# Performance work log

Hardware: AMD Instinct MI355X
Metric: run time of the kernel (lower is better)

Reference implementation:

```python
import jax, jax.numpy as jnp
import numpy as np

E = 1024   # embed_dim
H = 16     # num_heads
DH = E // H
FF = 4096  # intermediate_size
EPS = 1e-5


def layernorm(x, g, b):
    mu = jnp.mean(x, axis=-1, keepdims=True)
    var = jnp.var(x, axis=-1, keepdims=True)
    return (x - mu) * jax.lax.rsqrt(var + EPS) * g + b


def setup_inputs() -> dict:
    key = jax.random.key(0)
    ks = jax.random.split(key, 16)
    s = 0.02
    return {
        "x": jax.random.normal(ks[0], (2, 2048, E), dtype=jnp.float32),
        "ln1_g": jnp.ones((E,), jnp.float32),
        "ln1_b": jnp.zeros((E,), jnp.float32),
        "ln2_g": jnp.ones((E,), jnp.float32),
        "ln2_b": jnp.zeros((E,), jnp.float32),
        # per-head Q/K/V projections stacked: [H, E, DH]
        "wq": jax.random.normal(ks[1], (H, E, DH), jnp.float32) * s,
        "bq": jnp.zeros((H, DH), jnp.float32),
        "wk": jax.random.normal(ks[2], (H, E, DH), jnp.float32) * s,
        "bk": jnp.zeros((H, DH), jnp.float32),
        "wv": jax.random.normal(ks[3], (H, E, DH), jnp.float32) * s,
        "bv": jnp.zeros((H, DH), jnp.float32),
        "wo": jax.random.normal(ks[4], (E, E), jnp.float32) * s,
        "bo": jnp.zeros((E,), jnp.float32),
        "w1": jax.random.normal(ks[5], (E, FF), jnp.float32) * s,
        "b1": jnp.zeros((FF,), jnp.float32),
        "w2": jax.random.normal(ks[6], (FF, E), jnp.float32) * s,
        "b2": jnp.zeros((E,), jnp.float32),
    }


def reference(x, ln1_g, ln1_b, ln2_g, ln2_b, wq, bq, wk, bk, wv, bv,
              wo, bo, w1, b1, w2, b2):
    # --- multi-head attention (pre-LN) ---
    h = layernorm(x, ln1_g, ln1_b)                       # [B,S,E]
    q = jnp.einsum('bse,hed->bhsd', h, wq) + bq[:, None, :]
    k = jnp.einsum('bse,hed->bhsd', h, wk) + bk[:, None, :]
    v = jnp.einsum('bse,hed->bhsd', h, wv) + bv[:, None, :]
    scores = jnp.einsum('bhsd,bhtd->bhst', q, k) / jnp.sqrt(
        jnp.asarray(DH, x.dtype))                        # [B,H,S,S]
    w = jax.nn.softmax(scores, axis=-1)
    attn = jnp.einsum('bhst,bhtd->bhsd', w, v)           # [B,H,S,DH]
    B, _, S, _ = attn.shape
    concat = attn.transpose(0, 2, 1, 3).reshape(B, S, E)  # head concat order
    x = x + concat @ wo + bo
    # --- feed-forward (pre-LN), exact GELU, dropout_p=0 ---
    h2 = layernorm(x, ln2_g, ln2_b)
    ff = jax.nn.gelu(h2 @ w1 + b1, approximate=False) @ w2 + b2
    return x + ff
```

## Files before the change

### kernel.cpp

```cpp
#include <hip/hip_runtime.h>
#include <hip/hip_bf16.h>
#include <math.h>

typedef __attribute__((ext_vector_type(8))) short short8;
typedef __attribute__((ext_vector_type(4))) float f32x4;
typedef __attribute__((ext_vector_type(16))) float f32x16;
typedef __attribute__((ext_vector_type(4))) unsigned u32x4;

#define MFMA_BF16(a, b, c) __builtin_amdgcn_mfma_f32_16x16x32_bf16(a, b, c, 0, 0, 0)
#define MFMA32_BF16(a, b, c) __builtin_amdgcn_mfma_f32_32x32x16_bf16(a, b, c, 0, 0, 0)

#define GLD_LDS16(g, l)                                              \
  __builtin_amdgcn_global_load_lds(                                  \
      (const __attribute__((address_space(1))) void*)(g),            \
      (__attribute__((address_space(3))) void*)(l), 16, 0, 0)

__device__ __forceinline__ unsigned cvt_pk_bf16(float lo, float hi) {
  unsigned r;
  asm("v_cvt_pk_bf16_f32 %0, %1, %2" : "=v"(r) : "v"(lo), "v"(hi));
  return r;
}
#define PSWAP(a, b) asm volatile("v_permlane32_swap_b32 %0, %1" : "+v"(a), "+v"(b))

__device__ __forceinline__ unsigned short f2bf(float f) {
  union { float f; unsigned u; } v; v.f = f;
  unsigned r = v.u + 0x7FFFu + ((v.u >> 16) & 1u);
  return (unsigned short)(r >> 16);
}

__global__ __launch_bounds__(256) void transpose_cast(
    const float* __restrict__ in, unsigned short* __restrict__ out,
    int R, int C, size_t in_bs, size_t out_bs) {
  __shared__ float t[32][33];
  const float* inp = in + blockIdx.z * in_bs;
  unsigned short* outp = out + blockIdx.z * out_bs;
  const int c0 = blockIdx.x * 32, r0 = blockIdx.y * 32;
  const int tx = threadIdx.x, ty = threadIdx.y;
#pragma unroll
  for (int i = 0; i < 32; i += 8)
    t[ty + i][tx] = inp[(size_t)(r0 + ty + i) * C + c0 + tx];
  __syncthreads();
#pragma unroll
  for (int i = 0; i < 32; i += 8)
    outp[(size_t)(c0 + ty + i) * R + r0 + tx] = f2bf(t[tx][ty + i]);
}

__global__ void concat_bias(const float* __restrict__ bq, const float* __restrict__ bk,
                            const float* __restrict__ bv, float* __restrict__ bcat) {
  int i = blockIdx.x * 256 + threadIdx.x;
  if (i < 1024) bcat[i] = bq[i];
  else if (i < 2048) bcat[i] = bk[i - 1024];
  else if (i < 3072) bcat[i] = bv[i - 2048];
}

__global__ __launch_bounds__(256) void ln_kernel(
    const float* __restrict__ x, const float* __restrict__ g,
    const float* __restrict__ bb, unsigned short* __restrict__ out) {
  const int row = blockIdx.x, tid = threadIdx.x;
  const float4 v = ((const float4*)(x + (size_t)row * 1024))[tid];
  float s = v.x + v.y + v.z + v.w;
  float ss = v.x * v.x + v.y * v.y + v.z * v.z + v.w * v.w;
#pragma unroll
  for (int k = 1; k < 64; k <<= 1) {
    s += __shfl_xor(s, k, 64);
    ss += __shfl_xor(ss, k, 64);
  }
  __shared__ float red[8];
  const int wid = tid >> 6;
  if ((tid & 63) == 0) { red[wid] = s; red[wid + 4] = ss; }
  __syncthreads();
  s = red[0] + red[1] + red[2] + red[3];
  ss = red[4] + red[5] + red[6] + red[7];
  const float mu = s * (1.0f / 1024.0f);
  const float var = ss * (1.0f / 1024.0f) - mu * mu;
  const float rs = rsqrtf(var + 1e-5f);
  const float4 gv = ((const float4*)g)[tid];
  const float4 bv = ((const float4*)bb)[tid];
  ushort4 o;
  o.x = f2bf((v.x - mu) * rs * gv.x + bv.x);
  o.y = f2bf((v.y - mu) * rs * gv.y + bv.y);
  o.z = f2bf((v.z - mu) * rs * gv.z + bv.z);
  o.w = f2bf((v.w - mu) * rs * gv.w + bv.w);
  ((ushort4*)(out + (size_t)row * 1024))[tid] = o;
}

template <int EPI, int BN>
__global__ __launch_bounds__(256, 2) void gemm_bt(
    const unsigned short* __restrict__ A, const unsigned short* __restrict__ Bt,
    const float* __restrict__ bias, const float* __restrict__ res,
    void* __restrict__ Cout, int M, int N, int K) {
  constexpr int NFR = BN / 32;
  constexpr int BISS = BN / 32;
  __shared__ unsigned short As[128 * 64];
  __shared__ unsigned short Bs[BN * 64];
  const int tid = threadIdx.x;
  const int wid = tid >> 6, lane = tid & 63;
  const int li = lane & 15, gi = lane >> 4;
  const int bm = blockIdx.y, bn = blockIdx.x;
  const int wr = (wid >> 1) << 6;
  const int wc = (wid & 1) * (BN / 2);

  f32x4 acc[4][NFR];
#pragma unroll
  for (int m = 0; m < 4; ++m)
#pragma unroll
    for (int n = 0; n < NFR; ++n) acc[m][n] = (f32x4)0.0f;

  const size_t Ksz = (size_t)K;
  const int srow = tid >> 3;
  const int segG = (tid & 7) ^ (srow & 7);
  const unsigned short* Ab = A + (size_t)(bm * 128 + srow) * Ksz + segG * 8;
  const unsigned short* Bb = Bt + (size_t)(bn * BN + srow) * Ksz + segG * 8;

  for (int kt = 0; kt < K; kt += 64) {
#pragma unroll
    for (int c = 0; c < 4; ++c)
      GLD_LDS16(Ab + (size_t)(c * 32) * Ksz + kt, As + c * 2048 + wid * 512);
#pragma unroll
    for (int c = 0; c < BISS; ++c)
      GLD_LDS16(Bb + (size_t)(c * 32) * Ksz + kt, Bs + c * 2048 + wid * 512);
    __syncthreads();
    short8 af[4][2], bf[NFR][2];
#pragma unroll
    for (int m = 0; m < 4; ++m)
#pragma unroll
      for (int kk = 0; kk < 2; ++kk) {
        const int row = wr + m * 16 + li;
        af[m][kk] = *(const short8*)(As + row * 64 + ((kk * 4 + gi) ^ (row & 7)) * 8);
      }
#pragma unroll
    for (int n = 0; n < NFR; ++n)
#pragma unroll
      for (int kk = 0; kk < 2; ++kk) {
        const int row = wc + n * 16 + li;
        bf[n][kk] = *(const short8*)(Bs + row * 64 + ((kk * 4 + gi) ^ (row & 7)) * 8);
      }
    __builtin_amdgcn_s_setprio(1);
#pragma unroll
    for (int m = 0; m < 4; ++m)
#pragma unroll
      for (int n = 0; n < NFR; ++n) {
        acc[m][n] = MFMA_BF16(af[m][0], bf[n][0], acc[m][n]);
        acc[m][n] = MFMA_BF16(af[m][1], bf[n][1], acc[m][n]);
      }
    __builtin_amdgcn_s_setprio(0);
    __syncthreads();
  }

  const int row_base = bm * 128 + wr + gi * 4;
  const int col_base = bn * BN + wc + li;
#pragma unroll
  for (int m = 0; m < 4; ++m) {
#pragma unroll
    for (int n = 0; n < NFR; ++n) {
      const int col = col_base + n * 16;
      const float bi = bias[col];
#pragma unroll
      for (int r = 0; r < 4; ++r) {
        const int row = row_base + m * 16 + r;
        float v = acc[m][n][r] + bi;
        if (EPI == 2) v = 0.5f * v * (1.0f + erff(v * 0.70710678118654752f));
        const size_t idx = (size_t)row * N + col;
        if (EPI == 1) ((float*)Cout)[idx] = v + res[idx];
        else ((unsigned short*)Cout)[idx] = f2bf(v);
      }
    }
  }
}

__global__ __launch_bounds__(512, 2) void attn_kernel(
    const unsigned short* __restrict__ qkv, unsigned short* __restrict__ outp) {
  __shared__ unsigned short Kl[2][4096];
  __shared__ unsigned VT[2][64 * 33];
  __shared__ float Lb[8][32];
  const int tid = threadIdx.x;
  const int wid = tid >> 6, lane = tid & 63;
  const int l31 = lane & 31, hiq = lane >> 5;
  const int b = blockIdx.z, h = blockIdx.y;
  const int q0 = blockIdx.x * 256 + wid * 32;
  const int LD = 3072;
  const size_t base = (size_t)b * 2048 * LD;

  short8 qb[4];
  {
    const unsigned short* qp = qkv + base + (size_t)(q0 + l31) * LD + h * 64 + hiq * 8;
#pragma unroll
    for (int ds = 0; ds < 4; ++ds) qb[ds] = *(const short8*)(qp + ds * 16);
  }

  f32x16 o0 = (f32x16)0.0f, o1 = (f32x16)0.0f;
  float l_ = 0.0f;

  const int krow = wid * 8 + (lane >> 3);
  const int ksegG = (lane & 7) ^ (krow & 7);
  const unsigned short* kdma = qkv + base + 1024 + h * 64 + ksegG * 8 + (size_t)krow * LD;

  const int kp = tid >> 4, dq = tid & 15;
  const unsigned short* vsrc = qkv + base + 2048 + h * 64 + dq * 4 + (size_t)(2 * kp) * LD;

  auto kstage = [&](int buf, int t) {
    GLD_LDS16(kdma + (size_t)t * 64 * LD, &Kl[buf][wid * 512]);
  };

  kstage(0, 0);
  {
    const ushort4 a = *(const ushort4*)(vsrc);
    const ushort4 c = *(const ushort4*)(vsrc + LD);
    VT[0][(dq * 4 + 0) * 33 + kp] = (unsigned)a.x | ((unsigned)c.x << 16);
    VT[0][(dq * 4 + 1) * 33 + kp] = (unsigned)a.y | ((unsigned)c.y << 16);
    VT[0][(dq * 4 + 2) * 33 + kp] = (unsigned)a.z | ((unsigned)c.z << 16);
    VT[0][(dq * 4 + 3) * 33 + kp] = (unsigned)a.w | ((unsigned)c.w << 16);
  }
  __syncthreads();

  for (int t = 0; t < 32; ++t) {
    ushort4 va{}, vc{};
    if (t < 31) {
      kstage((t + 1) & 1, t + 1);
      const unsigned short* vs = vsrc + (size_t)(t + 1) * 64 * LD;
      va = *(const ushort4*)(vs);
      vc = *(const ushort4*)(vs + LD);
    }

    const unsigned short* kl = Kl[t & 1];
    short8 kf[2][4];
#pragma unroll
    for (int kvb = 0; kvb < 2; ++kvb)
#pragma unroll
      for (int ds = 0; ds < 4; ++ds)
        kf[kvb][ds] = *(const short8*)(
            kl + (kvb * 32 + l31) * 64 + (((2 * ds + hiq) ^ (lane & 7)) * 8));

    f32x16 sA = (f32x16)0.0f, sB = (f32x16)0.0f;
    __builtin_amdgcn_s_setprio(1);
#pragma unroll
    for (int ds = 0; ds < 4; ++ds) {
      sA = MFMA32_BF16(kf[0][ds], qb[ds], sA);
      sB = MFMA32_BF16(kf[1][ds], qb[ds], sB);
    }
    __builtin_amdgcn_s_setprio(0);

    const unsigned short* vtb = (const unsigned short*)VT[t & 1];
#pragma unroll
    for (int kvb = 0; kvb < 2; ++kvb) {
      const f32x16 s = kvb ? sB : sA;
      unsigned P[8];
#pragma unroll
      for (int i = 0; i < 8; ++i) {
        const float pe = __expf(s[2 * i] * 0.125f);
        const float po = __expf(s[2 * i + 1] * 0.125f);
        l_ += pe + po;
        P[i] = cvt_pk_bf16(pe, po);
      }
      PSWAP(P[0], P[2]); PSWAP(P[1], P[3]);
      PSWAP(P[4], P[6]); PSWAP(P[5], P[7]);
      const short8 pa0 = __builtin_bit_cast(short8, (u32x4){P[0], P[1], P[2], P[3]});
      const short8 pa1 = __builtin_bit_cast(short8, (u32x4){P[4], P[5], P[6], P[7]});
      const int ks0 = 2 * kvb;
      const short8 v00 = *(const short8*)(vtb + (0 * 32 + l31) * 66 + (8 * ks0 + 4 * hiq) * 2);
      const short8 v01 = *(const short8*)(vtb + (0 * 32 + l31) * 66 + (8 * ks0 + 8 + 4 * hiq) * 2);
      const short8 v10 = *(const short8*)(vtb + (1 * 32 + l31) * 66 + (8 * ks0 + 4 * hiq) * 2);
      const short8 v11 = *(const short8*)(vtb + (1 * 32 + l31) * 66 + (8 * ks0 + 8 + 4 * hiq) * 2);
      __builtin_amdgcn_s_setprio(1);
      o0 = MFMA32_BF16(pa0, v00, o0);
      o0 = MFMA32_BF16(pa1, v01, o0);
      o1 = MFMA32_BF16(pa0, v10, o1);
      o1 = MFMA32_BF16(pa1, v11, o1);
      __builtin_amdgcn_s_setprio(0);
    }

    if (t < 31) {
      unsigned* vd = VT[(t + 1) & 1];
      vd[(dq * 4 + 0) * 33 + kp] = (unsigned)va.x | ((unsigned)vc.x << 16);
      vd[(dq * 4 + 1) * 33 + kp] = (unsigned)va.y | ((unsigned)vc.y << 16);
      vd[(dq * 4 + 2) * 33 + kp] = (unsigned)va.z | ((unsigned)vc.z << 16);
      vd[(dq * 4 + 3) * 33 + kp] = (unsigned)va.w | ((unsigned)vc.w << 16);
    }
    __syncthreads();
  }

  const float lt = l_ + __shfl_xor(l_, 32, 64);
  Lb[wid][l31] = 1.0f / lt;
#pragma unroll
  for (int r = 0; r < 16; ++r) {
    const int crow = (r & 3) + 8 * (r >> 2) + 4 * hiq;
    const float inv = Lb[wid][crow];
    const size_t rowb = (size_t)(b * 2048 + q0 + crow) * 1024 + h * 64 + l31;
    outp[rowb]      = f2bf(o0[r] * inv);
    outp[rowb + 32] = f2bf(o1[r] * inv);
  }
}

extern "C" void kernel_launch(void* const* d_in, const int* in_sizes, int n_in,
                              void* d_out, int out_size, void* d_ws, size_t ws_size,
                              hipStream_t stream) {
  const float* x     = (const float*)d_in[0];
  const float* ln1_g = (const float*)d_in[1];
  const float* ln1_b = (const float*)d_in[2];
  const float* ln2_g = (const float*)d_in[3];
  const float* ln2_b = (const float*)d_in[4];
  const float* wq    = (const float*)d_in[5];
  const float* bq    = (const float*)d_in[6];
  const float* wk    = (const float*)d_in[7];
  const float* bk    = (const float*)d_in[8];
  const float* wv    = (const float*)d_in[9];
  const float* bv    = (const float*)d_in[10];
  const float* wo    = (const float*)d_in[11];
  const float* bo    = (const float*)d_in[12];
  const float* w1    = (const float*)d_in[13];
  const float* b1    = (const float*)d_in[14];
  const float* w2    = (const float*)d_in[15];
  const float* b2    = (const float*)d_in[16];
  float* out = (float*)d_out;

  char* p = (char*)d_ws;
  unsigned short* ws_h     = (unsigned short*)p; p += 4096ull * 1024 * 2;
  unsigned short* ws_qkv   = (unsigned short*)p; p += 4096ull * 3072 * 2;
  unsigned short* ws_attn  = (unsigned short*)p; p += 4096ull * 1024 * 2;
  unsigned short* ws_wqkvT = (unsigned short*)p; p += 3072ull * 1024 * 2;
  unsigned short* ws_woT   = (unsigned short*)p; p += 1024ull * 1024 * 2;
  unsigned short* ws_w1T   = (unsigned short*)p; p += 4096ull * 1024 * 2;
  unsigned short* ws_w2T   = (unsigned short*)p; p += 1024ull * 4096 * 2;
  float*          ws_bqkv  = (float*)p;          p += 3072 * 4;
  unsigned short* ws_ff = ws_qkv;

  const dim3 tb(32, 8);
  transpose_cast<<<dim3(2, 32, 16), tb, 0, stream>>>(
      wq, ws_wqkvT, 1024, 64, (size_t)(1024 * 64), (size_t)(64 * 1024));
  transpose_cast<<<dim3(2, 32, 16), tb, 0, stream>>>(
      wk, ws_wqkvT + 1024ull * 1024, 1024, 64, (size_t)(1024 * 64), (size_t)(64 * 1024));
  transpose_cast<<<dim3(2, 32, 16), tb, 0, stream>>>(
      wv, ws_wqkvT + 2048ull * 1024, 1024, 64, (size_t)(1024 * 64), (size_t)(64 * 1024));
  transpose_cast<<<dim3(32, 32, 1), tb, 0, stream>>>(wo, ws_woT, 1024, 1024, 0, 0);
  transpose_cast<<<dim3(128, 32, 1), tb, 0, stream>>>(w1, ws_w1T, 1024, 4096, 0, 0);
  transpose_cast<<<dim3(32, 128, 1), tb, 0, stream>>>(w2, ws_w2T, 4096, 1024, 0, 0);
  concat_bias<<<12, 256, 0, stream>>>(bq, bk, bv, ws_bqkv);

  ln_kernel<<<4096, 256, 0, stream>>>(x, ln1_g, ln1_b, ws_h);
  gemm_bt<0, 128><<<dim3(24, 32), 256, 0, stream>>>(ws_h, ws_wqkvT, ws_bqkv, nullptr,
                                                    ws_qkv, 4096, 3072, 1024);
  attn_kernel<<<dim3(8, 16, 2), 512, 0, stream>>>(ws_qkv, ws_attn);
  gemm_bt<1, 64><<<dim3(16, 32), 256, 0, stream>>>(ws_attn, ws_woT, bo, x,
                                                   out, 4096, 1024, 1024);
  ln_kernel<<<4096, 256, 0, stream>>>(out, ln2_g, ln2_b, ws_h);
  gemm_bt<2, 128><<<dim3(32, 32), 256, 0, stream>>>(ws_h, ws_w1T, b1, nullptr,
                                                    ws_ff, 4096, 4096, 1024);
  gemm_bt<1, 64><<<dim3(16, 32), 256, 0, stream>>>(ws_ff, ws_w2T, b2, out,
                                                   out, 4096, 1024, 4096);
}
```

Before: 290.6 us.

## Split attention over KV halves with a combine kernel and smaller blocks

```diff
diff --git a/kernel.cpp b/kernel.cpp
--- a/kernel.cpp
+++ b/kernel.cpp
@@ -26,6 +26,10 @@
   union { float f; unsigned u; } v; v.f = f;
   unsigned r = v.u + 0x7FFFu + ((v.u >> 16) & 1u);
   return (unsigned short)(r >> 16);
+}
+__device__ __forceinline__ float bf2f(unsigned short u) {
+  union { unsigned u; float f; } v; v.u = ((unsigned)u) << 16;
+  return v.f;
 }
 
 __global__ __launch_bounds__(256) void transpose_cast(
@@ -85,7 +89,7 @@
 }
 
 template <int EPI, int BN>
-__global__ __launch_bounds__(256, 2) void gemm_bt(
+__global__ __launch_bounds__(256, 3) void gemm_bt(
     const unsigned short* __restrict__ A, const unsigned short* __restrict__ Bt,
     const float* __restrict__ bias, const float* __restrict__ res,
     void* __restrict__ Cout, int M, int N, int K) {
@@ -168,18 +172,19 @@
   }
 }
 
-__global__ __launch_bounds__(512, 2) void attn_kernel(
-    const unsigned short* __restrict__ qkv, unsigned short* __restrict__ outp) {
+__global__ __launch_bounds__(256, 4) void attn_kernel(
+    const unsigned short* __restrict__ qkv, unsigned short* __restrict__ op0,
+    unsigned short* __restrict__ op1, float* __restrict__ lpart) {
   __shared__ unsigned short Kl[2][4096];
   __shared__ unsigned VT[2][64 * 33];
-  __shared__ float Lb[8][32];
   const int tid = threadIdx.x;
   const int wid = tid >> 6, lane = tid & 63;
   const int l31 = lane & 31, hiq = lane >> 5;
-  const int b = blockIdx.z, h = blockIdx.y;
-  const int q0 = blockIdx.x * 256 + wid * 32;
+  const int kvh = blockIdx.z & 1, b = blockIdx.z >> 1, h = blockIdx.y;
+  const int q0 = blockIdx.x * 128 + wid * 32;
   const int LD = 3072;
   const size_t base = (size_t)b * 2048 * LD;
+  const size_t kvoff = (size_t)kvh * 1024 * LD;
 
   short8 qb[4];
   {
@@ -189,37 +194,40 @@
   }
 
   f32x16 o0 = (f32x16)0.0f, o1 = (f32x16)0.0f;
-  float l_ = 0.0f;
-
-  const int krow = wid * 8 + (lane >> 3);
-  const int ksegG = (lane & 7) ^ (krow & 7);
-  const unsigned short* kdma = qkv + base + 1024 + h * 64 + ksegG * 8 + (size_t)krow * LD;
-
-  const int kp = tid >> 4, dq = tid & 15;
-  const unsigned short* vsrc = qkv + base + 2048 + h * 64 + dq * 4 + (size_t)(2 * kp) * LD;
+  float la = 0.0f, lb = 0.0f;
+
+  const int krw = lane >> 3;
+  const int ksegG = (lane & 7) ^ krw;
+  const unsigned short* kdma = qkv + base + kvoff + 1024 + h * 64 + ksegG * 8 +
+                               (size_t)(wid * 16 + krw) * LD;
+
+  const int kp = tid >> 3, dq8 = tid & 7;
+  const unsigned short* vsrc = qkv + base + kvoff + 2048 + h * 64 + dq8 * 8 +
+                               (size_t)(2 * kp) * LD;
 
   auto kstage = [&](int buf, int t) {
-    GLD_LDS16(kdma + (size_t)t * 64 * LD, &Kl[buf][wid * 512]);
+    GLD_LDS16(kdma + (size_t)t * 64 * LD, &Kl[buf][wid * 1024]);
+    GLD_LDS16(kdma + (size_t)(t * 64 + 8) * LD, &Kl[buf][wid * 1024 + 512]);
   };
+  auto vwrite = [&](int buf, short8 a, short8 c) {
+    unsigned* vd = VT[buf];
+#pragma unroll
+    for (int j = 0; j < 8; ++j)
+      vd[(dq8 * 8 + j) * 33 + kp] =
+          (unsigned)(unsigned short)a[j] | ((unsigned)(unsigned short)c[j] << 16);
+  };
 
   kstage(0, 0);
-  {
-    const ushort4 a = *(const ushort4*)(vsrc);
-    const ushort4 c = *(const ushort4*)(vsrc + LD);
-    VT[0][(dq * 4 + 0) * 33 + kp] = (unsigned)a.x | ((unsigned)c.x << 16);
-    VT[0][(dq * 4 + 1) * 33 + kp] = (unsigned)a.y | ((unsigned)c.y << 16);
-    VT[0][(dq * 4 + 2) * 33 + kp] = (unsigned)a.z | ((unsigned)c.z << 16);
-    VT[0][(dq * 4 + 3) * 33 + kp] = (unsigned)a.w | ((unsigned)c.w << 16);
-  }
+  vwrite(0, *(const short8*)vsrc, *(const short8*)(vsrc + LD));
   __syncthreads();
 
-  for (int t = 0; t < 32; ++t) {
-    ushort4 va{}, vc{};
-    if (t < 31) {
+  for (int t = 0; t < 16; ++t) {
+    short8 va{}, vc{};
+    if (t < 15) {
       kstage((t + 1) & 1, t + 1);
       const unsigned short* vs = vsrc + (size_t)(t + 1) * 64 * LD;
-      va = *(const ushort4*)(vs);
-      vc = *(const ushort4*)(vs + LD);
+      va = *(const short8*)(vs);
+      vc = *(const short8*)(vs + LD);
     }
 
     const unsigned short* kl = Kl[t & 1];
@@ -229,7 +237,7 @@
 #pragma unroll
       for (int ds = 0; ds < 4; ++ds)
         kf[kvb][ds] = *(const short8*)(
-            kl + (kvb * 32 + l31) * 64 + (((2 * ds + hiq) ^ (lane & 7)) * 8));
+            kl + (kvb * 32 + l31) * 64 + (((2 * ds + hiq) ^ (l31 & 7)) * 8));
 
     f32x16 sA = (f32x16)0.0f, sB = (f32x16)0.0f;
     __builtin_amdgcn_s_setprio(1);
@@ -249,7 +257,7 @@
       for (int i = 0; i < 8; ++i) {
         const float pe = __expf(s[2 * i] * 0.125f);
         const float po = __expf(s[2 * i + 1] * 0.125f);
-        l_ += pe + po;
+        la += pe; lb += po;
         P[i] = cvt_pk_bf16(pe, po);
       }
       PSWAP(P[0], P[2]); PSWAP(P[1], P[3]);
@@ -269,26 +277,38 @@
       __builtin_amdgcn_s_setprio(0);
     }
 
-    if (t < 31) {
-      unsigned* vd = VT[(t + 1) & 1];
-      vd[(dq * 4 + 0) * 33 + kp] = (unsigned)va.x | ((unsigned)vc.x << 16);
-      vd[(dq * 4 + 1) * 33 + kp] = (unsigned)va.y | ((unsigned)vc.y << 16);
-      vd[(dq * 4 + 2) * 33 + kp] = (unsigned)va.z | ((unsigned)vc.z << 16);
-      vd[(dq * 4 + 3) * 33 + kp] = (unsigned)va.w | ((unsigned)vc.w << 16);
-    }
+    if (t < 15) vwrite((t + 1) & 1, va, vc);
     __syncthreads();
   }
 
-  const float lt = l_ + __shfl_xor(l_, 32, 64);
-  Lb[wid][l31] = 1.0f / lt;
+  const float lsum = la + lb;
+  const float lt = lsum + __shfl_xor(lsum, 32, 64);
+  if (hiq == 0)
+    lpart[(size_t)kvh * 65536 + ((size_t)(b * 2048 + q0 + l31) * 16) + h] = lt;
+
+  unsigned short* op = kvh ? op1 : op0;
 #pragma unroll
   for (int r = 0; r < 16; ++r) {
     const int crow = (r & 3) + 8 * (r >> 2) + 4 * hiq;
-    const float inv = Lb[wid][crow];
     const size_t rowb = (size_t)(b * 2048 + q0 + crow) * 1024 + h * 64 + l31;
-    outp[rowb]      = f2bf(o0[r] * inv);
-    outp[rowb + 32] = f2bf(o1[r] * inv);
-  }
+    op[rowb]      = f2bf(o0[r]);
+    op[rowb + 32] = f2bf(o1[r]);
+  }
+}
+
+__global__ __launch_bounds__(256) void attn_combine(
+    const unsigned short* __restrict__ op0, unsigned short* __restrict__ op1io,
+    const float* __restrict__ lpart) {
+  const size_t i8 = (size_t)blockIdx.x * 256 + threadIdx.x;
+  const size_t g = (i8 * 8) >> 6;
+  const float inv = 1.0f / (lpart[g] + lpart[g + 65536]);
+  const short8 a = *(const short8*)(op0 + i8 * 8);
+  const short8 c = *(const short8*)(op1io + i8 * 8);
+  short8 o;
+#pragma unroll
+  for (int j = 0; j < 8; ++j)
+    o[j] = (short)f2bf((bf2f((unsigned short)a[j]) + bf2f((unsigned short)c[j])) * inv);
+  *(short8*)(op1io + i8 * 8) = o;
 }
 
 extern "C" void kernel_launch(void* const* d_in, const int* in_sizes, int n_in,
@@ -322,6 +342,7 @@
   unsigned short* ws_w1T   = (unsigned short*)p; p += 4096ull * 1024 * 2;
   unsigned short* ws_w2T   = (unsigned short*)p; p += 1024ull * 4096 * 2;
   float*          ws_bqkv  = (float*)p;          p += 3072 * 4;
+  float*          ws_l     = (float*)p;          p += 2ull * 65536 * 4;
   unsigned short* ws_ff = ws_qkv;
 
   const dim3 tb(32, 8);
@@ -339,7 +360,8 @@
   ln_kernel<<<4096, 256, 0, stream>>>(x, ln1_g, ln1_b, ws_h);
   gemm_bt<0, 128><<<dim3(24, 32), 256, 0, stream>>>(ws_h, ws_wqkvT, ws_bqkv, nullptr,
                                                     ws_qkv, 4096, 3072, 1024);
-  attn_kernel<<<dim3(8, 16, 2), 512, 0, stream>>>(ws_qkv, ws_attn);
+  attn_kernel<<<dim3(16, 16, 4), 256, 0, stream>>>(ws_qkv, ws_h, ws_attn, ws_l);
+  attn_combine<<<2048, 256, 0, stream>>>(ws_h, ws_attn, ws_l);
   gemm_bt<1, 64><<<dim3(16, 32), 256, 0, stream>>>(ws_attn, ws_woT, bo, x,
                                                    out, 4096, 1024, 1024);
   ln_kernel<<<4096, 256, 0, stream>>>(out, ln2_g, ln2_b, ws_h);
```

Result: faster. 284.7 us (-2.0%).
